# Optimization experiments

Measured on AMD Instinct MI355X. Metric: run time of the kernel, lower is better.

## Reference

```python
import jax, jax.numpy as jnp
import numpy as np

THRESHOLD = 8.0
BN_EPS = 1e-5


def setup_inputs() -> dict:
    key = jax.random.key(0)
    k1, k2 = jax.random.split(key)
    B, C, H, W = 2, 128, 64, 64
    x = jax.random.normal(k1, (B, C, H, W), dtype=jnp.float32)
    W_fc = jax.random.normal(k2, (C, C), dtype=jnp.float32) * (1.0 / np.sqrt(C))
    b_fc = jnp.zeros((C,), dtype=jnp.float32)
    gamma = jnp.ones((C,), dtype=jnp.float32)
    beta = jnp.zeros((C,), dtype=jnp.float32)
    return {"x": x, "W_fc": W_fc, "b_fc": b_fc, "gamma": gamma, "beta": beta}


def _mean_agg(X, path):
    # X: [B,N,C], path: [B,N,N] (col->row). out = rownorm(path) @ X
    out = jnp.matmul(path, X)
    s = jnp.sum(path, axis=2, keepdims=True)  # [B,N,1]
    norm = jnp.where(s > 0, 1.0 / s, 0.0)     # inf -> 0 as in torch code
    return norm * out


def reference(x, W_fc, b_fc, gamma, beta):
    b, c, h, w = x.shape
    N = h * w
    # [B,N,C] token features
    xf = jnp.transpose(x.reshape(b, c, N), (0, 2, 1))
    # pairwise euclidean distance (cdist, p=2)
    sq = jnp.sum(xf * xf, axis=-1)  # [B,N]
    d2 = sq[:, :, None] + sq[:, None, :] - 2.0 * jnp.einsum('bnc,bmc->bnm', xf, xf)
    dist = jnp.sqrt(jnp.maximum(d2, 0.0))
    Hg = (dist < THRESHOLD).astype(xf.dtype)  # [B,N,N] hypergraph incidence
    # HyperGraphConv: y = fc(x); E = mean(H^T @ y); out = mean(H @ E); res = y + out
    y = jnp.einsum('bnc,dc->bnd', xf, W_fc) + b_fc
    E = _mean_agg(y, jnp.swapaxes(Hg, 1, 2))
    x_out = _mean_agg(E, Hg)
    xe = y + x_out  # [B,N,C]
    # back to [B,C,H,W]
    xo = jnp.transpose(xe, (0, 2, 1)).reshape(b, c, h, w)
    # BatchNorm2d (training mode: batch stats over B,H,W) + SiLU
    mean = jnp.mean(xo, axis=(0, 2, 3), keepdims=True)
    var = jnp.var(xo, axis=(0, 2, 3), keepdims=True)
    xn = (xo - mean) * jax.lax.rsqrt(var + BN_EPS)
    xn = gamma[None, :, None, None] * xn + beta[None, :, None, None]
    return xn * jax.nn.sigmoid(xn)
```

## Files before the change

### kernel.cpp

```cpp
#include <hip/hip_runtime.h>
#include <hip/hip_cooperative_groups.h>

namespace cg = cooperative_groups;

typedef unsigned short ushort_t;
typedef unsigned int   uint32;
typedef unsigned long long u64;
typedef __bf16 bf16_t;
typedef bf16_t bf16x8 __attribute__((ext_vector_type(8)));
typedef float  f32x4  __attribute__((ext_vector_type(4)));

#define N_TOK 4096
#define C_DIM 128
#define NTOT  8192
#define THRESH2 64.0f
#define NBLK 512

#define XF_OFF  (0u)
#define YF_OFF  (2u<<20)
#define EF_OFF  (6u<<20)
#define XE_OFF  (10u<<20)
#define SQ_OFF  (14u<<20)
#define BN_OFF  ((14u<<20) + 32768u)
#define HB_OFF  (16u<<20)
#define WS_NEED ((size_t)(24u<<20))

__device__ __forceinline__ float b2f(ushort_t u){ return __uint_as_float(((uint32)u)<<16); }
__device__ __forceinline__ ushort_t f2b(float f){
    uint32 u = __float_as_uint(f);
    u += 0x7fffu + ((u>>16)&1u);
    return (ushort_t)(u>>16);
}
__device__ __forceinline__ u64 shfl_u64(u64 v, int src){
    uint32 lo = (uint32)v, hi = (uint32)(v>>32);
    lo = __shfl(lo, src); hi = __shfl(hi, src);
    return ((u64)hi<<32)|lo;
}
__device__ __forceinline__ u64 shfl_xor_u64(u64 v, int m){
    uint32 lo = (uint32)v, hi = (uint32)(v>>32);
    lo = __shfl_xor(lo, m); hi = __shfl_xor(hi, m);
    return ((u64)hi<<32)|lo;
}

union SMem {
    struct { ushort_t Xs[64*136]; ushort_t Ws[64*136]; } fc;
    struct { ushort_t Al[128*136]; ushort_t Bl[64*136]; u64 rowW[128]; u64 part[256]; } gr;
    struct { float r1[4][128]; float r2[4][128]; } agg;
    struct { float tile[32][33]; } bn;
};

__global__ __launch_bounds__(256, 2) void k_fused(const float* __restrict__ x,
                                                  const float* __restrict__ W,
                                                  const float* __restrict__ bfc,
                                                  const float* __restrict__ gamma,
                                                  const float* __restrict__ beta,
                                                  ushort_t* __restrict__ Xf,
                                                  float* __restrict__ Yf,
                                                  float* __restrict__ Ef,
                                                  float* __restrict__ Xe,
                                                  float* __restrict__ sq,
                                                  float* __restrict__ bnp,
                                                  u64* __restrict__ Hb,
                                                  float* __restrict__ out){
    __shared__ SMem sm;
    cg::grid_group grid = cg::this_grid();
    int tid = threadIdx.x;
    int bid = blockIdx.x;

    if (bid < 256){
        int t0 = (bid >> 1) * 64;
        int dh = bid & 1;
        int b  = t0 >> 12;
        int n0 = t0 & 4095;
        if (bid == 0){
            #pragma unroll
            for (int k=0;k<8;k++) bnp[tid + 256*k] = 0.f;
        }
        const float* xb = x + (size_t)b * C_DIM * N_TOK + n0;
        #pragma unroll
        for (int k=0;k<8;k++){
            int idx = tid + 256*k;
            int c = idx >> 4, n4 = (idx & 15)*4;
            float4 v = *(const float4*)(xb + (size_t)c*N_TOK + n4);
            sm.fc.Xs[(n4+0)*136 + c] = f2b(v.x);
            sm.fc.Xs[(n4+1)*136 + c] = f2b(v.y);
            sm.fc.Xs[(n4+2)*136 + c] = f2b(v.z);
            sm.fc.Xs[(n4+3)*136 + c] = f2b(v.w);
        }
        const float* Wb = W + (size_t)dh*64*C_DIM;
        #pragma unroll
        for (int k=0;k<8;k++){
            int idx = tid + 256*k;
            int d = idx >> 5, c4 = (idx & 31)*4;
            float4 v = *(const float4*)(Wb + d*C_DIM + c4);
            uint2 u;
            u.x = (uint32)f2b(v.x) | ((uint32)f2b(v.y)<<16);
            u.y = (uint32)f2b(v.z) | ((uint32)f2b(v.w)<<16);
            *(uint2*)(&sm.fc.Ws[d*136 + c4]) = u;
        }
        __syncthreads();
        #pragma unroll
        for (int k=0;k<2;k++){
            int idx = tid + 256*(k + 2*dh);
            int row = idx >> 4, c8 = (idx & 15)*8;
            uint4 o = *(const uint4*)(&sm.fc.Xs[row*136 + c8]);
            *(uint4*)(Xf + (size_t)(t0 + row)*C_DIM + c8) = o;
        }
        if (dh == 0){
            int tok = tid >> 2, p = tid & 3;
            const ushort_t* xr = &sm.fc.Xs[tok*136 + p*32];
            float sacc = 0.f;
            #pragma unroll
            for (int i=0;i<16;i++){
                uint32 u = *(const uint32*)(&xr[i*2]);
                float v0 = __uint_as_float(u<<16);
                float v1 = __uint_as_float(u & 0xffff0000u);
                sacc = fmaf(v0, v0, sacc);
                sacc = fmaf(v1, v1, sacc);
            }
            sacc += __shfl_xor(sacc, 1);
            sacc += __shfl_xor(sacc, 2);
            if (p == 0) sq[t0 + tok] = sacc;
        }
        int wv = tid >> 6, lane = tid & 63;
        int qd = lane >> 4, m = lane & 15;
        f32x4 acc[4] = {{0,0,0,0},{0,0,0,0},{0,0,0,0},{0,0,0,0}};
        #pragma unroll
        for (int kc=0;kc<4;kc++){
            bf16x8 af = *(const bf16x8*)(&sm.fc.Xs[(wv*16 + m)*136 + kc*32 + qd*8]);
            #pragma unroll
            for (int ct=0;ct<4;ct++){
                bf16x8 bfr = *(const bf16x8*)(&sm.fc.Ws[(ct*16+m)*136 + kc*32 + qd*8]);
                acc[ct] = __builtin_amdgcn_mfma_f32_16x16x32_bf16(af, bfr, acc[ct], 0, 0, 0);
            }
        }
        int row = t0 + wv*16 + qd*4;
        #pragma unroll
        for (int ct=0;ct<4;ct++){
            int d = dh*64 + ct*16 + m;
            float bias = bfc[d];
            #pragma unroll
            for (int r=0;r<4;r++)
                Yf[(size_t)(row + r)*C_DIM + d] = acc[ct][r] + bias;
        }
    }
    grid.sync();

    for (int item = bid; item < 2112; item += NBLK){
        __syncthreads();
        int bb = (item >= 1056) ? 1 : 0;
        int L = item - bb*1056;
        int bi = (int)((65.0f - sqrtf(4225.0f - 4.0f*(float)L)) * 0.5f);
        while (bi > 0 && bi*(65-bi) > L) --bi;
        while ((bi+1)*(65-(bi+1)) <= L) ++bi;
        int bj = L - bi*(65-bi) + 2*bi;
        int i0 = bi*128, j0 = bj*64;
        const ushort_t* XfA = Xf + (size_t)(bb*N_TOK + i0)*C_DIM;
        const ushort_t* XfB = Xf + (size_t)(bb*N_TOK + j0)*C_DIM;
        #pragma unroll
        for (int k=0;k<8;k++){
            int q = tid + 256*k;
            int row = q >> 4, cp = (q & 15)*8;
            *(uint4*)(&sm.gr.Al[row*136 + cp]) = *(const uint4*)(XfA + row*C_DIM + cp);
        }
        #pragma unroll
        for (int k=0;k<4;k++){
            int q = tid + 256*k;
            int row = q >> 4, cp = (q & 15)*8;
            *(uint4*)(&sm.gr.Bl[row*136 + cp]) = *(const uint4*)(XfB + row*C_DIM + cp);
        }
        __syncthreads();
        int wv = tid >> 6, lane = tid & 63;
        int qd = lane >> 4, m = lane & 15;
        f32x4 acc[2][4] = {{{0,0,0,0},{0,0,0,0},{0,0,0,0},{0,0,0,0}},
                           {{0,0,0,0},{0,0,0,0},{0,0,0,0},{0,0,0,0}}};
        #pragma unroll
        for (int kc=0;kc<4;kc++){
            bf16x8 a0 = *(const bf16x8*)(&sm.gr.Al[(wv*32 +      m)*136 + kc*32 + qd*8]);
            bf16x8 a1 = *(const bf16x8*)(&sm.gr.Al[(wv*32 + 16 + m)*136 + kc*32 + qd*8]);
            #pragma unroll
            for (int ct=0;ct<4;ct++){
                bf16x8 bfr = *(const bf16x8*)(&sm.gr.Bl[(ct*16+m)*136 + kc*32 + qd*8]);
                acc[0][ct] = __builtin_amdgcn_mfma_f32_16x16x32_bf16(a0, bfr, acc[0][ct], 0, 0, 0);
                acc[1][ct] = __builtin_amdgcn_mfma_f32_16x16x32_bf16(a1, bfr, acc[1][ct], 0, 0, 0);
            }
        }
        float sqj[4];
        #pragma unroll
        for (int ct=0;ct<4;ct++) sqj[ct] = sq[bb*N_TOK + j0 + ct*16 + m];
        #pragma unroll
        for (int rt=0;rt<2;rt++){
            int lr = wv*32 + rt*16 + qd*4;
            int ib = i0 + lr;
            float sqi[4];
            #pragma unroll
            for (int r=0;r<4;r++) sqi[r] = sq[bb*N_TOK + ib + r];
            #pragma unroll
            for (int r=0;r<4;r++){
                u64 bits = 0;
                #pragma unroll
                for (int ct=0;ct<4;ct++){
                    float d2 = sqi[r] + sqj[ct] - 2.0f*acc[rt][ct][r];
                    if (d2 < THRESH2) bits |= (u64)1 << (ct*16 + m);
                }
                bits |= shfl_xor_u64(bits, 1);
                bits |= shfl_xor_u64(bits, 2);
                bits |= shfl_xor_u64(bits, 4);
                bits |= shfl_xor_u64(bits, 8);
                if (m == 0){
                    Hb[(size_t)(bb*N_TOK + ib + r)*64 + bj] = bits;
                    sm.gr.rowW[lr + r] = bits;
                }
            }
        }
        __syncthreads();
        {
            int jj = tid & 63, hw = (tid>>6)&1, sub = tid>>7;
            u64 p = 0;
            int ibase = hw*64 + sub*32;
            #pragma unroll 8
            for (int ii=0; ii<32; ii++){
                u64 wrd = sm.gr.rowW[ibase + ii];
                p |= ((wrd >> jj) & 1ull) << (sub*32 + ii);
            }
            sm.gr.part[tid] = p;
        }
        __syncthreads();
        if (tid < 128){
            int jj = tid & 63, hw = tid >> 6;
            u64 wt = sm.gr.part[tid] | sm.gr.part[tid + 128];
            Hb[(size_t)(bb*N_TOK + j0 + jj)*64 + 2*bi + hw] = wt;
        }
    }
    grid.sync();

    {
        int wv = tid >> 6, lane = tid & 63;
        u64 myw[4];
        float nrm[4];
        #pragma unroll
        for (int k=0;k<4;k++){
            int row = (bid + k*NBLK)*4 + wv;
            u64 w = Hb[(size_t)row*64 + lane];
            myw[k] = w;
            int cnt = __builtin_popcountll(w);
            cnt += __shfl_xor(cnt, 1);
            cnt += __shfl_xor(cnt, 2);
            cnt += __shfl_xor(cnt, 4);
            cnt += __shfl_xor(cnt, 8);
            cnt += __shfl_xor(cnt, 16);
            cnt += __shfl_xor(cnt, 32);
            nrm[k] = (cnt > 0) ? 1.0f/(float)cnt : 0.0f;
        }
        #pragma unroll
        for (int k=0;k<4;k++){
            int row = (bid + k*NBLK)*4 + wv;
            int b = row >> 12;
            const float* Vb = Yf + (size_t)b*N_TOK*C_DIM;
            float acc0 = 0.f, acc1 = 0.f;
            u64 nz = __ballot(myw[k] != 0);
            while (nz){
                int wdi = __builtin_ctzll(nz);
                nz &= nz - 1;
                u64 mw = shfl_u64(myw[k], wdi);
                while (mw){
                    int j = wdi*64 + __builtin_ctzll(mw);
                    mw &= mw - 1;
                    acc0 += Vb[(size_t)j*C_DIM + lane];
                    acc1 += Vb[(size_t)j*C_DIM + lane + 64];
                }
            }
            size_t o = (size_t)row*C_DIM;
            Ef[o + lane]      = acc0*nrm[k];
            Ef[o + lane + 64] = acc1*nrm[k];
        }
        grid.sync();
        float s1a=0.f, s1b=0.f, s2a=0.f, s2b=0.f;
        #pragma unroll
        for (int k=0;k<4;k++){
            int row = (bid + k*NBLK)*4 + wv;
            int b = row >> 12;
            const float* Vb = Ef + (size_t)b*N_TOK*C_DIM;
            float acc0 = 0.f, acc1 = 0.f;
            u64 nz = __ballot(myw[k] != 0);
            while (nz){
                int wdi = __builtin_ctzll(nz);
                nz &= nz - 1;
                u64 mw = shfl_u64(myw[k], wdi);
                while (mw){
                    int j = wdi*64 + __builtin_ctzll(mw);
                    mw &= mw - 1;
                    acc0 += Vb[(size_t)j*C_DIM + lane];
                    acc1 += Vb[(size_t)j*C_DIM + lane + 64];
                }
            }
            size_t o = (size_t)row*C_DIM;
            float xe0 = Yf[o + lane]      + acc0*nrm[k];
            float xe1 = Yf[o + lane + 64] + acc1*nrm[k];
            Xe[o + lane]      = xe0;
            Xe[o + lane + 64] = xe1;
            s1a += xe0; s2a += xe0*xe0;
            s1b += xe1; s2b += xe1*xe1;
        }
        __syncthreads();
        sm.agg.r1[wv][lane]      = s1a;
        sm.agg.r1[wv][lane + 64] = s1b;
        sm.agg.r2[wv][lane]      = s2a;
        sm.agg.r2[wv][lane + 64] = s2b;
        __syncthreads();
        if (tid < 128){
            float s1 = sm.agg.r1[0][tid]+sm.agg.r1[1][tid]+sm.agg.r1[2][tid]+sm.agg.r1[3][tid];
            float s2 = sm.agg.r2[0][tid]+sm.agg.r2[1][tid]+sm.agg.r2[2][tid]+sm.agg.r2[3][tid];
            int prt = bid & 7;
            atomicAdd(&bnp[prt*256 + tid],       s1);
            atomicAdd(&bnp[prt*256 + 128 + tid], s2);
        }
    }
    grid.sync();

    for (int it = bid; it < 1024; it += NBLK){
        __syncthreads();
        int bx = it & 127, byz = it >> 7;
        int by = byz & 3, bz = byz >> 2;
        int tx = tid & 31, ty = tid >> 5;
        int n0 = bx*32, c0 = by*32, b = bz;
        int c = c0 + tx;
        float s1 = 0.f, s2 = 0.f;
        #pragma unroll
        for (int p=0;p<8;p++){
            s1 += bnp[p*256 + c];
            s2 += bnp[p*256 + 128 + c];
        }
        float inv = 1.0f / (float)NTOT;
        float mean = s1 * inv;
        float var  = s2*inv - mean*mean;
        float scale = gamma[c] * rsqrtf(var + 1e-5f);
        float shift = beta[c] - mean*scale;
        #pragma unroll
        for (int k=0;k<4;k++){
            int nl = ty + 8*k;
            float v = Xe[(size_t)(b*N_TOK + n0 + nl)*C_DIM + c];
            v = scale*v + shift;
            float sg = 1.0f/(1.0f + __expf(-v));
            sm.bn.tile[tx][nl] = v * sg;
        }
        __syncthreads();
        #pragma unroll
        for (int k=0;k<4;k++){
            int cl = ty + 8*k;
            out[(size_t)(b*C_DIM + c0 + cl)*N_TOK + n0 + tx] = sm.bn.tile[cl][tx];
        }
    }
}

__global__ __launch_bounds__(256) void k_fc(const float* __restrict__ x,
                                            const float* __restrict__ W,
                                            const float* __restrict__ bfc,
                                            ushort_t* __restrict__ Xf,
                                            float* __restrict__ Yf,
                                            float* __restrict__ sq,
                                            float* __restrict__ bnp){
    __shared__ ushort_t Xs[64*136];
    __shared__ ushort_t Ws[64*136];
    int tid = threadIdx.x;
    int t0 = blockIdx.x * 64;
    int dh = blockIdx.y;
    int b  = t0 >> 12;
    int n0 = t0 & 4095;
    if (blockIdx.x == 0 && dh == 0){
        #pragma unroll
        for (int k=0;k<8;k++) bnp[tid + 256*k] = 0.f;
    }
    const float* xb = x + (size_t)b * C_DIM * N_TOK + n0;
    #pragma unroll
    for (int k=0;k<8;k++){
        int idx = tid + 256*k;
        int c = idx >> 4, n4 = (idx & 15)*4;
        float4 v = *(const float4*)(xb + (size_t)c*N_TOK + n4);
        Xs[(n4+0)*136 + c] = f2b(v.x);
        Xs[(n4+1)*136 + c] = f2b(v.y);
        Xs[(n4+2)*136 + c] = f2b(v.z);
        Xs[(n4+3)*136 + c] = f2b(v.w);
    }
    const float* Wb = W + (size_t)dh*64*C_DIM;
    #pragma unroll
    for (int k=0;k<8;k++){
        int idx = tid + 256*k;
        int d = idx >> 5, c4 = (idx & 31)*4;
        float4 v = *(const float4*)(Wb + d*C_DIM + c4);
        uint2 u;
        u.x = (uint32)f2b(v.x) | ((uint32)f2b(v.y)<<16);
        u.y = (uint32)f2b(v.z) | ((uint32)f2b(v.w)<<16);
        *(uint2*)(&Ws[d*136 + c4]) = u;
    }
    __syncthreads();
    #pragma unroll
    for (int k=0;k<2;k++){
        int idx = tid + 256*(k + 2*dh);
        int row = idx >> 4, c8 = (idx & 15)*8;
        uint4 o = *(const uint4*)(&Xs[row*136 + c8]);
        *(uint4*)(Xf + (size_t)(t0 + row)*C_DIM + c8) = o;
    }
    if (dh == 0){
        int tok = tid >> 2, p = tid & 3;
        const ushort_t* xr = &Xs[tok*136 + p*32];
        float sacc = 0.f;
        #pragma unroll
        for (int i=0;i<16;i++){
            uint32 u = *(const uint32*)(&xr[i*2]);
            float v0 = __uint_as_float(u<<16);
            float v1 = __uint_as_float(u & 0xffff0000u);
            sacc = fmaf(v0, v0, sacc);
            sacc = fmaf(v1, v1, sacc);
        }
        sacc += __shfl_xor(sacc, 1);
        sacc += __shfl_xor(sacc, 2);
        if (p == 0) sq[t0 + tok] = sacc;
    }
    int wv = tid >> 6, lane = tid & 63;
    int qd = lane >> 4, m = lane & 15;
    f32x4 acc[4] = {{0,0,0,0},{0,0,0,0},{0,0,0,0},{0,0,0,0}};
    #pragma unroll
    for (int kc=0;kc<4;kc++){
        bf16x8 af = *(const bf16x8*)(&Xs[(wv*16 + m)*136 + kc*32 + qd*8]);
        #pragma unroll
        for (int ct=0;ct<4;ct++){
            bf16x8 bfr = *(const bf16x8*)(&Ws[(ct*16+m)*136 + kc*32 + qd*8]);
            acc[ct] = __builtin_amdgcn_mfma_f32_16x16x32_bf16(af, bfr, acc[ct], 0, 0, 0);
        }
    }
    int row = t0 + wv*16 + qd*4;
    #pragma unroll
    for (int ct=0;ct<4;ct++){
        int d = dh*64 + ct*16 + m;
        float bias = bfc[d];
        #pragma unroll
        for (int r=0;r<4;r++)
            Yf[(size_t)(row + r)*C_DIM + d] = acc[ct][r] + bias;
    }
}

__global__ __launch_bounds__(256) void k_gram(const ushort_t* __restrict__ Xf,
                                              const float* __restrict__ sq,
                                              u64* __restrict__ Hb){
    __shared__ ushort_t Al[128*136];
    __shared__ ushort_t Bl[64*136];
    __shared__ u64 rowW[128];
    __shared__ u64 part[256];
    int tid = threadIdx.x;
    int L = blockIdx.x, b = blockIdx.y;
    int bi = (int)((65.0f - sqrtf(4225.0f - 4.0f*(float)L)) * 0.5f);
    while (bi > 0 && bi*(65-bi) > L) --bi;
    while ((bi+1)*(65-(bi+1)) <= L) ++bi;
    int bj = L - bi*(65-bi) + 2*bi;
    int i0 = bi*128, j0 = bj*64;
    const ushort_t* XfA = Xf + (size_t)(b*N_TOK + i0)*C_DIM;
    const ushort_t* XfB = Xf + (size_t)(b*N_TOK + j0)*C_DIM;
    #pragma unroll
    for (int k=0;k<8;k++){
        int q = tid + 256*k;
        int row = q >> 4, cp = (q & 15)*8;
        *(uint4*)(&Al[row*136 + cp]) = *(const uint4*)(XfA + row*C_DIM + cp);
    }
    #pragma unroll
    for (int k=0;k<4;k++){
        int q = tid + 256*k;
        int row = q >> 4, cp = (q & 15)*8;
        *(uint4*)(&Bl[row*136 + cp]) = *(const uint4*)(XfB + row*C_DIM + cp);
    }
    __syncthreads();
    int wv = tid >> 6, lane = tid & 63;
    int qd = lane >> 4, m = lane & 15;
    f32x4 acc[2][4] = {{{0,0,0,0},{0,0,0,0},{0,0,0,0},{0,0,0,0}},
                       {{0,0,0,0},{0,0,0,0},{0,0,0,0},{0,0,0,0}}};
    #pragma unroll
    for (int kc=0;kc<4;kc++){
        bf16x8 a0 = *(const bf16x8*)(&Al[(wv*32 +      m)*136 + kc*32 + qd*8]);
        bf16x8 a1 = *(const bf16x8*)(&Al[(wv*32 + 16 + m)*136 + kc*32 + qd*8]);
        #pragma unroll
        for (int ct=0;ct<4;ct++){
            bf16x8 bfr = *(const bf16x8*)(&Bl[(ct*16+m)*136 + kc*32 + qd*8]);
            acc[0][ct] = __builtin_amdgcn_mfma_f32_16x16x32_bf16(a0, bfr, acc[0][ct], 0, 0, 0);
            acc[1][ct] = __builtin_amdgcn_mfma_f32_16x16x32_bf16(a1, bfr, acc[1][ct], 0, 0, 0);
        }
    }
    float sqj[4];
    #pragma unroll
    for (int ct=0;ct<4;ct++) sqj[ct] = sq[b*N_TOK + j0 + ct*16 + m];
    #pragma unroll
    for (int rt=0;rt<2;rt++){
        int lr = wv*32 + rt*16 + qd*4;
        int ib = i0 + lr;
        float sqi[4];
        #pragma unroll
        for (int r=0;r<4;r++) sqi[r] = sq[b*N_TOK + ib + r];
        #pragma unroll
        for (int r=0;r<4;r++){
            u64 bits = 0;
            #pragma unroll
            for (int ct=0;ct<4;ct++){
                float d2 = sqi[r] + sqj[ct] - 2.0f*acc[rt][ct][r];
                if (d2 < THRESH2) bits |= (u64)1 << (ct*16 + m);
            }
            bits |= shfl_xor_u64(bits, 1);
            bits |= shfl_xor_u64(bits, 2);
            bits |= shfl_xor_u64(bits, 4);
            bits |= shfl_xor_u64(bits, 8);
            if (m == 0){
                Hb[(size_t)(b*N_TOK + ib + r)*64 + bj] = bits;
                rowW[lr + r] = bits;
            }
        }
    }
    __syncthreads();
    {
        int jj = tid & 63, hw = (tid>>6)&1, sub = tid>>7;
        u64 p = 0;
        int ibase = hw*64 + sub*32;
        #pragma unroll 8
        for (int ii=0; ii<32; ii++){
            u64 wrd = rowW[ibase + ii];
            p |= ((wrd >> jj) & 1ull) << (sub*32 + ii);
        }
        part[tid] = p;
    }
    __syncthreads();
    if (tid < 128){
        int jj = tid & 63, hw = tid >> 6;
        u64 wt = part[tid] | part[tid + 128];
        Hb[(size_t)(b*N_TOK + j0 + jj)*64 + 2*bi + hw] = wt;
    }
}

template<int MODE>
__global__ __launch_bounds__(256) void k_aggs(const u64* __restrict__ Hb,
                                              const float* __restrict__ V,
                                              const float* __restrict__ Yf,
                                              float* __restrict__ Out,
                                              float* __restrict__ bnp){
    __shared__ float r1[4][128];
    __shared__ float r2[4][128];
    int tid = threadIdx.x;
    int wv = tid >> 6, lane = tid & 63;
    int row = blockIdx.x * 4 + wv;
    int b = row >> 12;
    u64 myw = Hb[(size_t)row*64 + lane];
    int cnt = __builtin_popcountll(myw);
    cnt += __shfl_xor(cnt, 1);
    cnt += __shfl_xor(cnt, 2);
    cnt += __shfl_xor(cnt, 4);
    cnt += __shfl_xor(cnt, 8);
    cnt += __shfl_xor(cnt, 16);
    cnt += __shfl_xor(cnt, 32);
    float acc0 = 0.f, acc1 = 0.f;
    const float* Vb = V + (size_t)b*N_TOK*C_DIM;
    u64 nz = __ballot(myw != 0);
    while (nz){
        int wdi = __builtin_ctzll(nz);
        nz &= nz - 1;
        u64 mw = shfl_u64(myw, wdi);
        while (mw){
            int j = wdi*64 + __builtin_ctzll(mw);
            mw &= mw - 1;
            acc0 += Vb[(size_t)j*C_DIM + lane];
            acc1 += Vb[(size_t)j*C_DIM + lane + 64];
        }
    }
    float norm = (cnt > 0) ? (1.0f/(float)cnt) : 0.0f;
    size_t o = (size_t)row*C_DIM;
    if (MODE == 0){
        Out[o + lane]      = acc0*norm;
        Out[o + lane + 64] = acc1*norm;
    } else {
        float xe0 = Yf[o + lane]      + acc0*norm;
        float xe1 = Yf[o + lane + 64] + acc1*norm;
        Out[o + lane]      = xe0;
        Out[o + lane + 64] = xe1;
        r1[wv][lane]      = xe0;
        r1[wv][lane + 64] = xe1;
        r2[wv][lane]      = xe0*xe0;
        r2[wv][lane + 64] = xe1*xe1;
        __syncthreads();
        if (tid < 128){
            float s1 = r1[0][tid]+r1[1][tid]+r1[2][tid]+r1[3][tid];
            float s2 = r2[0][tid]+r2[1][tid]+r2[2][tid]+r2[3][tid];
            int prt = blockIdx.x & 7;
            atomicAdd(&bnp[prt*256 + tid],       s1);
            atomicAdd(&bnp[prt*256 + 128 + tid], s2);
        }
    }
}

__global__ __launch_bounds__(256) void k_out(const float* __restrict__ Xe,
                                             const float* __restrict__ bnp,
                                             const float* __restrict__ gamma,
                                             const float* __restrict__ beta,
                                             float* __restrict__ out){
    __shared__ float tile[32][33];
    int tx = threadIdx.x, ty = threadIdx.y;
    int n0 = blockIdx.x*32, c0 = blockIdx.y*32, b = blockIdx.z;
    int c = c0 + tx;
    float s1 = 0.f, s2 = 0.f;
    #pragma unroll
    for (int p=0;p<8;p++){
        s1 += bnp[p*256 + c];
        s2 += bnp[p*256 + 128 + c];
    }
    float inv = 1.0f / (float)NTOT;
    float mean = s1 * inv;
    float var  = s2*inv - mean*mean;
    float scale = gamma[c] * rsqrtf(var + 1e-5f);
    float shift = beta[c] - mean*scale;
    #pragma unroll
    for (int k=0;k<4;k++){
        int nl = ty + 8*k;
        float v = Xe[(size_t)(b*N_TOK + n0 + nl)*C_DIM + c];
        v = scale*v + shift;
        float sg = 1.0f/(1.0f + __expf(-v));
        tile[tx][nl] = v * sg;
    }
    __syncthreads();
    #pragma unroll
    for (int k=0;k<4;k++){
        int cl = ty + 8*k;
        out[(size_t)(b*C_DIM + c0 + cl)*N_TOK + n0 + tx] = tile[cl][tx];
    }
}

extern "C" void kernel_launch(void* const* d_in, const int* in_sizes, int n_in,
                              void* d_out, int out_size, void* d_ws, size_t ws_size,
                              hipStream_t stream){
    if (ws_size < WS_NEED) return;
    const float* x     = (const float*)d_in[0];
    const float* W     = (const float*)d_in[1];
    const float* bfc   = (const float*)d_in[2];
    const float* gamma = (const float*)d_in[3];
    const float* beta  = (const float*)d_in[4];
    char* ws = (char*)d_ws;
    ushort_t* Xf = (ushort_t*)(ws + XF_OFF);
    float*    Yf = (float*)(ws + YF_OFF);
    float*    Ef = (float*)(ws + EF_OFF);
    float*    Xe = (float*)(ws + XE_OFF);
    float*    sqp= (float*)(ws + SQ_OFF);
    float*    bnp= (float*)(ws + BN_OFF);
    u64*      Hb = (u64*)(ws + HB_OFF);
    float*    outp = (float*)d_out;

    static int coop_ok = -1;
    if (coop_ok < 0){
        int ok = 0, dev = 0, nb = 0;
        if (hipGetDevice(&dev) == hipSuccess){
            hipDeviceProp_t prop;
            if (hipGetDeviceProperties(&prop, dev) == hipSuccess &&
                hipOccupancyMaxActiveBlocksPerMultiprocessor(&nb, (const void*)k_fused, 256, 0) == hipSuccess){
                ok = (prop.cooperativeLaunch != 0) && (nb * prop.multiProcessorCount >= NBLK);
            }
        }
        coop_ok = ok;
    }

    if (coop_ok){
        void* args[] = {(void*)&x, (void*)&W, (void*)&bfc, (void*)&gamma, (void*)&beta,
                        (void*)&Xf, (void*)&Yf, (void*)&Ef, (void*)&Xe, (void*)&sqp,
                        (void*)&bnp, (void*)&Hb, (void*)&outp};
        hipError_t e = hipLaunchCooperativeKernel((const void*)k_fused, dim3(NBLK), dim3(256),
                                                  args, 0, stream);
        if (e == hipSuccess) return;
    }

    k_fc<<<dim3(128,2), dim3(256), 0, stream>>>(x, W, bfc, Xf, Yf, sqp, bnp);
    k_gram<<<dim3(1056,2), dim3(256), 0, stream>>>(Xf, sqp, Hb);
    k_aggs<0><<<dim3(2048), dim3(256), 0, stream>>>(Hb, Yf, Yf, Ef, bnp);
    k_aggs<1><<<dim3(2048), dim3(256), 0, stream>>>(Hb, Ef, Yf, Xe, bnp);
    k_out<<<dim3(128,4,2), dim3(32,8), 0, stream>>>(Xe, bnp, gamma, beta, outp);
}
```

Baseline: 113.1 us.

## Double cooperative grid to 1024 blocks with 64x64 symmetric Gram tiles

Raises the persistent cooperative grid from 512 to 1024 blocks and the occupancy hint to 4 blocks per CU. To make room, the Gram/threshold stage now uses square 64x64 upper-triangular tiles, which roughly halves shared memory. Diagonal tiles skip the transposed bitmask write. The aggregation loops and the final BN loop are rescaled so each block handles fewer rows. The aim is more waves in flight to hide latency in the gather-heavy aggregation. The cost is more per-tile overhead, register pressure from the higher launch bound, and grid.sync spanning twice as many blocks.

```diff
diff --git a/kernel.cpp b/kernel.cpp
--- a/kernel.cpp
+++ b/kernel.cpp
@@ -14,7 +14,7 @@
 #define C_DIM 128
 #define NTOT  8192
 #define THRESH2 64.0f
-#define NBLK 512
+#define NBLK 1024
 
 #define XF_OFF  (0u)
 #define YF_OFF  (2u<<20)
@@ -25,7 +25,6 @@
 #define HB_OFF  (16u<<20)
 #define WS_NEED ((size_t)(24u<<20))
 
-__device__ __forceinline__ float b2f(ushort_t u){ return __uint_as_float(((uint32)u)<<16); }
 __device__ __forceinline__ ushort_t f2b(float f){
     uint32 u = __float_as_uint(f);
     u += 0x7fffu + ((u>>16)&1u);
@@ -44,12 +43,12 @@
 
 union SMem {
     struct { ushort_t Xs[64*136]; ushort_t Ws[64*136]; } fc;
-    struct { ushort_t Al[128*136]; ushort_t Bl[64*136]; u64 rowW[128]; u64 part[256]; } gr;
+    struct { ushort_t Al[64*136]; ushort_t Bl[64*136]; u64 rowW[64]; u64 part[256]; } gr;
     struct { float r1[4][128]; float r2[4][128]; } agg;
     struct { float tile[32][33]; } bn;
 };
 
-__global__ __launch_bounds__(256, 2) void k_fused(const float* __restrict__ x,
+__global__ __launch_bounds__(256, 4) void k_fused(const float* __restrict__ x,
                                                   const float* __restrict__ W,
                                                   const float* __restrict__ bfc,
                                                   const float* __restrict__ gamma,
@@ -146,100 +145,86 @@
     }
     grid.sync();
 
-    for (int item = bid; item < 2112; item += NBLK){
-        __syncthreads();
-        int bb = (item >= 1056) ? 1 : 0;
-        int L = item - bb*1056;
-        int bi = (int)((65.0f - sqrtf(4225.0f - 4.0f*(float)L)) * 0.5f);
-        while (bi > 0 && bi*(65-bi) > L) --bi;
-        while ((bi+1)*(65-(bi+1)) <= L) ++bi;
-        int bj = L - bi*(65-bi) + 2*bi;
-        int i0 = bi*128, j0 = bj*64;
+    for (int item = bid; item < 4160; item += NBLK){
+        __syncthreads();
+        int bb = (item >= 2080) ? 1 : 0;
+        int L = item - bb*2080;
+        int bi = (int)((129.0f - sqrtf(16641.0f - 8.0f*(float)L)) * 0.5f);
+        while (bi > 0 && bi*(129-bi)/2 > L) --bi;
+        while ((bi+1)*(129-(bi+1))/2 <= L) ++bi;
+        int bj = bi + (L - bi*(129-bi)/2);
+        int i0 = bi*64, j0 = bj*64;
         const ushort_t* XfA = Xf + (size_t)(bb*N_TOK + i0)*C_DIM;
         const ushort_t* XfB = Xf + (size_t)(bb*N_TOK + j0)*C_DIM;
         #pragma unroll
-        for (int k=0;k<8;k++){
+        for (int k=0;k<4;k++){
             int q = tid + 256*k;
             int row = q >> 4, cp = (q & 15)*8;
             *(uint4*)(&sm.gr.Al[row*136 + cp]) = *(const uint4*)(XfA + row*C_DIM + cp);
-        }
-        #pragma unroll
-        for (int k=0;k<4;k++){
-            int q = tid + 256*k;
-            int row = q >> 4, cp = (q & 15)*8;
             *(uint4*)(&sm.gr.Bl[row*136 + cp]) = *(const uint4*)(XfB + row*C_DIM + cp);
         }
         __syncthreads();
         int wv = tid >> 6, lane = tid & 63;
         int qd = lane >> 4, m = lane & 15;
-        f32x4 acc[2][4] = {{{0,0,0,0},{0,0,0,0},{0,0,0,0},{0,0,0,0}},
-                           {{0,0,0,0},{0,0,0,0},{0,0,0,0},{0,0,0,0}}};
+        f32x4 acc[4] = {{0,0,0,0},{0,0,0,0},{0,0,0,0},{0,0,0,0}};
         #pragma unroll
         for (int kc=0;kc<4;kc++){
-            bf16x8 a0 = *(const bf16x8*)(&sm.gr.Al[(wv*32 +      m)*136 + kc*32 + qd*8]);
-            bf16x8 a1 = *(const bf16x8*)(&sm.gr.Al[(wv*32 + 16 + m)*136 + kc*32 + qd*8]);
+            bf16x8 a0 = *(const bf16x8*)(&sm.gr.Al[(wv*16 + m)*136 + kc*32 + qd*8]);
             #pragma unroll
             for (int ct=0;ct<4;ct++){
                 bf16x8 bfr = *(const bf16x8*)(&sm.gr.Bl[(ct*16+m)*136 + kc*32 + qd*8]);
-                acc[0][ct] = __builtin_amdgcn_mfma_f32_16x16x32_bf16(a0, bfr, acc[0][ct], 0, 0, 0);
-                acc[1][ct] = __builtin_amdgcn_mfma_f32_16x16x32_bf16(a1, bfr, acc[1][ct], 0, 0, 0);
+                acc[ct] = __builtin_amdgcn_mfma_f32_16x16x32_bf16(a0, bfr, acc[ct], 0, 0, 0);
             }
         }
         float sqj[4];
         #pragma unroll
         for (int ct=0;ct<4;ct++) sqj[ct] = sq[bb*N_TOK + j0 + ct*16 + m];
-        #pragma unroll
-        for (int rt=0;rt<2;rt++){
-            int lr = wv*32 + rt*16 + qd*4;
-            int ib = i0 + lr;
-            float sqi[4];
-            #pragma unroll
-            for (int r=0;r<4;r++) sqi[r] = sq[bb*N_TOK + ib + r];
-            #pragma unroll
-            for (int r=0;r<4;r++){
-                u64 bits = 0;
-                #pragma unroll
-                for (int ct=0;ct<4;ct++){
-                    float d2 = sqi[r] + sqj[ct] - 2.0f*acc[rt][ct][r];
-                    if (d2 < THRESH2) bits |= (u64)1 << (ct*16 + m);
-                }
-                bits |= shfl_xor_u64(bits, 1);
-                bits |= shfl_xor_u64(bits, 2);
-                bits |= shfl_xor_u64(bits, 4);
-                bits |= shfl_xor_u64(bits, 8);
-                if (m == 0){
-                    Hb[(size_t)(bb*N_TOK + ib + r)*64 + bj] = bits;
-                    sm.gr.rowW[lr + r] = bits;
-                }
-            }
-        }
-        __syncthreads();
-        {
-            int jj = tid & 63, hw = (tid>>6)&1, sub = tid>>7;
+        int lr = wv*16 + qd*4;
+        int ib = i0 + lr;
+        float sqi[4];
+        #pragma unroll
+        for (int r=0;r<4;r++) sqi[r] = sq[bb*N_TOK + ib + r];
+        #pragma unroll
+        for (int r=0;r<4;r++){
+            u64 bits = 0;
+            #pragma unroll
+            for (int ct=0;ct<4;ct++){
+                float d2 = sqi[r] + sqj[ct] - 2.0f*acc[ct][r];
+                if (d2 < THRESH2) bits |= (u64)1 << (ct*16 + m);
+            }
+            bits |= shfl_xor_u64(bits, 1);
+            bits |= shfl_xor_u64(bits, 2);
+            bits |= shfl_xor_u64(bits, 4);
+            bits |= shfl_xor_u64(bits, 8);
+            if (m == 0){
+                Hb[(size_t)(bb*N_TOK + ib + r)*64 + bj] = bits;
+                sm.gr.rowW[lr + r] = bits;
+            }
+        }
+        __syncthreads();
+        if (bi != bj){
+            int jj = tid & 63, q = tid >> 6;
             u64 p = 0;
-            int ibase = hw*64 + sub*32;
-            #pragma unroll 8
-            for (int ii=0; ii<32; ii++){
-                u64 wrd = sm.gr.rowW[ibase + ii];
-                p |= ((wrd >> jj) & 1ull) << (sub*32 + ii);
-            }
+            int ibase = q*16;
+            #pragma unroll
+            for (int ii=0; ii<16; ii++)
+                p |= ((sm.gr.rowW[ibase + ii] >> jj) & 1ull) << (ibase + ii);
             sm.gr.part[tid] = p;
-        }
-        __syncthreads();
-        if (tid < 128){
-            int jj = tid & 63, hw = tid >> 6;
-            u64 wt = sm.gr.part[tid] | sm.gr.part[tid + 128];
-            Hb[(size_t)(bb*N_TOK + j0 + jj)*64 + 2*bi + hw] = wt;
+            __syncthreads();
+            if (tid < 64){
+                u64 wt = sm.gr.part[tid] | sm.gr.part[tid+64] | sm.gr.part[tid+128] | sm.gr.part[tid+192];
+                Hb[(size_t)(bb*N_TOK + j0 + tid)*64 + bi] = wt;
+            }
         }
     }
     grid.sync();
 
     {
         int wv = tid >> 6, lane = tid & 63;
-        u64 myw[4];
-        float nrm[4];
-        #pragma unroll
-        for (int k=0;k<4;k++){
+        u64 myw[2];
+        float nrm[2];
+        #pragma unroll
+        for (int k=0;k<2;k++){
             int row = (bid + k*NBLK)*4 + wv;
             u64 w = Hb[(size_t)row*64 + lane];
             myw[k] = w;
@@ -253,7 +238,7 @@
             nrm[k] = (cnt > 0) ? 1.0f/(float)cnt : 0.0f;
         }
         #pragma unroll
-        for (int k=0;k<4;k++){
+        for (int k=0;k<2;k++){
             int row = (bid + k*NBLK)*4 + wv;
             int b = row >> 12;
             const float* Vb = Yf + (size_t)b*N_TOK*C_DIM;
@@ -277,7 +262,7 @@
         grid.sync();
         float s1a=0.f, s1b=0.f, s2a=0.f, s2b=0.f;
         #pragma unroll
-        for (int k=0;k<4;k++){
+        for (int k=0;k<2;k++){
             int row = (bid + k*NBLK)*4 + wv;
             int b = row >> 12;
             const float* Vb = Ef + (size_t)b*N_TOK*C_DIM;
@@ -318,8 +303,8 @@
     }
     grid.sync();
 
-    for (int it = bid; it < 1024; it += NBLK){
-        __syncthreads();
+    {
+        int it = bid;
         int bx = it & 127, byz = it >> 7;
         int by = byz & 3, bz = byz >> 2;
         int tx = tid & 31, ty = tid >> 5;
```

Result: no change. 112.5 us (-0.6%).
